# Kernel optimization log

Hardware: AMD Instinct MI355X
Metric: run time of the kernel (lower is better)

## Reference

```python
import jax, jax.numpy as jnp
import numpy as np

B, H, W, C = 32, 56, 56, 192
NUM_HEADS = 6
WS = 7
SHIFT = 3
HIDDEN = 4 * C


def _relative_position_index(ws):
    coords = np.stack(np.meshgrid(np.arange(ws), np.arange(ws), indexing="ij"))  # 2,ws,ws
    coords = coords.reshape(2, -1)
    rel = coords[:, :, None] - coords[:, None, :]  # 2,N,N
    rel = rel.transpose(1, 2, 0)
    rel[:, :, 0] += ws - 1
    rel[:, :, 1] += ws - 1
    rel[:, :, 0] *= 2 * ws - 1
    return rel.sum(-1)  # N,N in [0, (2ws-1)^2)


def setup_inputs() -> dict:
    key = jax.random.key(0)
    ks = jax.random.split(key, 16)
    s = 0.02
    inp = {
        "x": jax.random.normal(ks[0], (B, H, W, C), jnp.float32),
        "norm1_g": jnp.ones((C,), jnp.float32),
        "norm1_b": jnp.zeros((C,), jnp.float32),
        "qkv_w": jax.random.normal(ks[1], (3 * C, C), jnp.float32) * s,
        "qkv_b": jnp.zeros((3 * C,), jnp.float32),
        "proj_w": jax.random.normal(ks[2], (C, C), jnp.float32) * s,
        "proj_b": jnp.zeros((C,), jnp.float32),
        "rel_bias_table": jax.random.normal(ks[3], ((2 * WS - 1) ** 2, NUM_HEADS), jnp.float32) * s,
        "norm2_g": jnp.ones((C,), jnp.float32),
        "norm2_b": jnp.zeros((C,), jnp.float32),
        "fc1_w": jax.random.normal(ks[4], (HIDDEN, C), jnp.float32) * s,
        "fc1_b": jnp.zeros((HIDDEN,), jnp.float32),
        "fc2_w": jax.random.normal(ks[5], (C, HIDDEN), jnp.float32) * s,
        "fc2_b": jnp.zeros((C,), jnp.float32),
        "rel_index": jnp.asarray(_relative_position_index(WS), jnp.int32),  # (49,49)
    }
    return inp


def _layernorm(x, g, b, eps=1e-5):
    mu = x.mean(-1, keepdims=True)
    var = ((x - mu) ** 2).mean(-1, keepdims=True)
    return (x - mu) * jax.lax.rsqrt(var + eps) * g + b


def _window_partition(x, ws):
    b, h, w, c = x.shape
    x = x.reshape(b, h // ws, ws, w // ws, ws, c)
    return x.transpose(0, 1, 3, 2, 4, 5).reshape(-1, ws * ws, c)


def _window_reverse(win, ws, b, h, w):
    c = win.shape[-1]
    x = win.reshape(b, h // ws, w // ws, ws, ws, c)
    return x.transpose(0, 1, 3, 2, 4, 5).reshape(b, h, w, c)


def reference(x, norm1_g, norm1_b, qkv_w, qkv_b, proj_w, proj_b, rel_bias_table,
              norm2_g, norm2_b, fc1_w, fc1_b, fc2_w, fc2_b, rel_index):
    shortcut = x
    xn = _layernorm(x, norm1_g, norm1_b)
    xs = jnp.roll(xn, (-SHIFT, -SHIFT), axis=(1, 2))
    win = _window_partition(xs, WS)  # (nW*B, 49, C)
    nw, n, c = win.shape
    hd = c // NUM_HEADS
    qkv = win @ qkv_w.T + qkv_b  # (nw, n, 3C)
    qkv = qkv.reshape(nw, n, 3, NUM_HEADS, hd).transpose(2, 0, 3, 1, 4)
    q, k, v = qkv[0], qkv[1], qkv[2]  # (nw, heads, n, hd)
    q = q * (hd ** -0.5)
    attn = jnp.einsum("whnd,whmd->whnm", q, k)
    bias = rel_bias_table[rel_index.reshape(-1)].reshape(n, n, NUM_HEADS).transpose(2, 0, 1)
    attn = jax.nn.softmax(attn + bias[None], axis=-1)
    out = jnp.einsum("whnm,whmd->whnd", attn, v)
    out = out.transpose(0, 2, 1, 3).reshape(nw, n, c)
    out = out @ proj_w.T + proj_b
    xs = _window_reverse(out, WS, x.shape[0], x.shape[1], x.shape[2])
    xa = jnp.roll(xs, (SHIFT, SHIFT), axis=(1, 2))
    x = shortcut + xa
    xm = _layernorm(x, norm2_g, norm2_b)
    xm = jax.nn.gelu(xm @ fc1_w.T + fc1_b, approximate=False)
    xm = xm @ fc2_w.T + fc2_b
    return x + xm
```

## Files before the change

### kernel.cpp

```cpp
#include <hip/hip_runtime.h>
#include <hip/hip_bf16.h>

#define CC 192
#define NHEADS 6
#define HDIM 32
#define NTOK 49
#define NWIN 2048
#define MTOK 100352
#define HIDDEN 768

typedef __hip_bfloat16 bf16;
typedef __attribute__((ext_vector_type(8))) short short8;
typedef __attribute__((ext_vector_type(4))) float f32x4;

__global__ __launch_bounds__(256) void k_wconv(
    const float* __restrict__ qw, const float* __restrict__ pw,
    const float* __restrict__ f1, const float* __restrict__ f2,
    bf16* __restrict__ o) {
  int i = blockIdx.x * 256 + threadIdx.x;
  if (i < 110592) o[i] = __float2bfloat16(qw[i]);
  else if (i < 147456) o[i] = __float2bfloat16(pw[i - 110592]);
  else if (i < 294912) o[i] = __float2bfloat16(f1[i - 147456]);
  else if (i < 442368) o[i] = __float2bfloat16(f2[i - 294912]);
}

__global__ __launch_bounds__(256) void k_bias(
    const float* __restrict__ table, const int* __restrict__ ridx,
    float* __restrict__ bias6) {
  int i = blockIdx.x * 256 + threadIdx.x;
  if (i >= 6 * 2401) return;
  int h = i / 2401, e = i - h * 2401;
  bias6[i] = table[ridx[e] * NHEADS + h];
}

__global__ __launch_bounds__(256) void k_ln1_part(
    const float* __restrict__ x, const float* __restrict__ g,
    const float* __restrict__ bta, bf16* __restrict__ xw) {
  int wv = blockIdx.x * 4 + (threadIdx.x >> 6);
  int lane = threadIdx.x & 63;
  int w = wv / NTOK, n = wv - w * NTOK;
  int b = w >> 6, wrem = w & 63;
  int hi = wrem >> 3, wi = wrem & 7;
  int i = n / 7, j = n - i * 7;
  int hsrc = hi * 7 + i + 3; if (hsrc >= 56) hsrc -= 56;
  int wsrc = wi * 7 + j + 3; if (wsrc >= 56) wsrc -= 56;
  const float* row = x + (size_t)((b * 56 + hsrc) * 56 + wsrc) * CC;
  float v0 = row[lane], v1 = row[lane + 64], v2 = row[lane + 128];
  float s = v0 + v1 + v2;
  for (int m = 32; m; m >>= 1) s += __shfl_xor(s, m, 64);
  float mu = s * (1.0f / 192.0f);
  float d0 = v0 - mu, d1 = v1 - mu, d2 = v2 - mu;
  float q = d0 * d0 + d1 * d1 + d2 * d2;
  for (int m = 32; m; m >>= 1) q += __shfl_xor(q, m, 64);
  float inv = rsqrtf(q * (1.0f / 192.0f) + 1e-5f);
  bf16* orow = xw + (size_t)wv * CC;
  orow[lane]       = __float2bfloat16(d0 * inv * g[lane]       + bta[lane]);
  orow[lane + 64]  = __float2bfloat16(d1 * inv * g[lane + 64]  + bta[lane + 64]);
  orow[lane + 128] = __float2bfloat16(d2 * inv * g[lane + 128] + bta[lane + 128]);
}

__global__ __launch_bounds__(256) void k_ln2(
    const float* __restrict__ x1, const float* __restrict__ g,
    const float* __restrict__ bta, bf16* __restrict__ xn2) {
  int wv = blockIdx.x * 4 + (threadIdx.x >> 6);
  int lane = threadIdx.x & 63;
  const float* row = x1 + (size_t)wv * CC;
  float v0 = row[lane], v1 = row[lane + 64], v2 = row[lane + 128];
  float s = v0 + v1 + v2;
  for (int m = 32; m; m >>= 1) s += __shfl_xor(s, m, 64);
  float mu = s * (1.0f / 192.0f);
  float d0 = v0 - mu, d1 = v1 - mu, d2 = v2 - mu;
  float q = d0 * d0 + d1 * d1 + d2 * d2;
  for (int m = 32; m; m >>= 1) q += __shfl_xor(q, m, 64);
  float inv = rsqrtf(q * (1.0f / 192.0f) + 1e-5f);
  bf16* orow = xn2 + (size_t)wv * CC;
  orow[lane]       = __float2bfloat16(d0 * inv * g[lane]       + bta[lane]);
  orow[lane + 64]  = __float2bfloat16(d1 * inv * g[lane + 64]  + bta[lane + 64]);
  orow[lane + 128] = __float2bfloat16(d2 * inv * g[lane + 128] + bta[lane + 128]);
}

template <int MODE, int NT, int KC, int MF>
__global__ __launch_bounds__(256) void k_gemm_areg(
    const bf16* __restrict__ A, const bf16* __restrict__ W,
    const float* __restrict__ bias, void* __restrict__ out0,
    const void* __restrict__ aux) {
  constexpr int K = KC * 192;
  constexpr int N = NT * 64;
  __shared__ bf16 Bs[2][64 * 192];
  const int tid = threadIdx.x;
  const int wave = tid >> 6, lane = tid & 63;
  const int grp = lane >> 4, rA = lane & 15;
  const int cq = grp, cn = rA;
  const int m0 = blockIdx.x * (MF * 64);
  const int mrow = m0 + wave * (MF * 16);

  short8 areg[MF][KC * 6];
#pragma unroll
  for (int mt = 0; mt < MF; ++mt) {
    const bf16* arow = A + (size_t)(mrow + mt * 16 + rA) * K + grp * 8;
#pragma unroll
    for (int kt = 0; kt < KC * 6; ++kt)
      areg[mt][kt] = *(const short8*)(arow + kt * 32);
  }

  int rowoff[MF][4];
  if (MODE == 1) {
#pragma unroll
    for (int mt = 0; mt < MF; ++mt)
#pragma unroll
      for (int r = 0; r < 4; ++r) {
        int m = mrow + mt * 16 + cq * 4 + r;
        int w = m / 49, rr = m - w * 49;
        int b = w >> 6, wrem = w & 63;
        int hi = wrem >> 3, wi = wrem & 7;
        int ii = rr / 7, jj = rr - ii * 7;
        int hd = hi * 7 + ii + 3; if (hd >= 56) hd -= 56;
        int wd = wi * 7 + jj + 3; if (wd >= 56) wd -= 56;
        rowoff[mt][r] = ((b * 56 + hd) * 56 + wd) * CC;
      }
  }

  auto stage = [&](int buf, int nt, int kc) {
#pragma unroll
    for (int i = 0; i < 6; ++i) {
      int c = i * 256 + tid;
      int row = c / 24;
      int cbl = ((c - row * 24) * 16) ^ ((row & 7) << 4);
      const char* src = (const char*)W +
          (size_t)(nt * 64 + row) * (K * 2) + kc * 384 + cbl;
      __builtin_amdgcn_global_load_lds(
          (const __attribute__((address_space(1))) void*)src,
          (__attribute__((address_space(3))) void*)((char*)&Bs[buf][0] + c * 16),
          16, 0, 0);
    }
  };
  stage(0, 0, 0);

  f32x4 acc[MF][4];
#pragma unroll
  for (int s = 0; s < NT * KC; ++s) {
    const int nt = s / KC, kc = s - nt * KC;
    const int cur = s & 1;
    __syncthreads();
    if (s + 1 < NT * KC) stage(cur ^ 1, (s + 1) / KC, (s + 1) % KC);
    if (kc == 0) {
#pragma unroll
      for (int mt = 0; mt < MF; ++mt)
#pragma unroll
        for (int ntf = 0; ntf < 4; ++ntf)
          acc[mt][ntf] = (f32x4){0.f, 0.f, 0.f, 0.f};
    }
#pragma unroll
    for (int kt = 0; kt < 6; ++kt) {
      short8 b[4];
#pragma unroll
      for (int ntf = 0; ntf < 4; ++ntf) {
        int row = ntf * 16 + rA;
        int phys = row * 384 + ((kt * 64 + grp * 16) ^ ((row & 7) << 4));
        b[ntf] = *(const short8*)((const char*)&Bs[cur][0] + phys);
      }
#pragma unroll
      for (int mt = 0; mt < MF; ++mt)
#pragma unroll
        for (int ntf = 0; ntf < 4; ++ntf)
          acc[mt][ntf] = __builtin_amdgcn_mfma_f32_16x16x32_bf16(
              areg[mt][kc * 6 + kt], b[ntf], acc[mt][ntf], 0, 0, 0);
    }
    if (kc == KC - 1) {
      const int n0t = nt * 64;
      float bi[4];
#pragma unroll
      for (int ntf = 0; ntf < 4; ++ntf) bi[ntf] = bias[n0t + ntf * 16 + cn];
#pragma unroll
      for (int mt = 0; mt < MF; ++mt) {
#pragma unroll
        for (int r = 0; r < 4; ++r) {
          const int m = mrow + mt * 16 + cq * 4 + r;
#pragma unroll
          for (int ntf = 0; ntf < 4; ++ntf) {
            const int n = n0t + ntf * 16 + cn;
            float v = acc[mt][ntf][r] + bi[ntf];
            if (MODE == 0) {
              ((bf16*)out0)[(size_t)m * N + n] = __float2bfloat16(v);
            } else if (MODE == 2) {
              float ge = 0.5f * v * (1.0f + erff(v * 0.70710678118654752f));
              ((bf16*)out0)[(size_t)m * N + n] = __float2bfloat16(ge);
            } else if (MODE == 1) {
              float res = ((const float*)aux)[(size_t)rowoff[mt][r] + n];
              ((float*)out0)[(size_t)rowoff[mt][r] + n] = v + res;
            } else {
              float res = ((const float*)aux)[(size_t)m * CC + n];
              ((float*)out0)[(size_t)m * CC + n] = v + res;
            }
          }
        }
      }
    }
  }
}

__global__ __launch_bounds__(256) void k_attn_mfma(
    const bf16* __restrict__ qk, const float* __restrict__ bias6,
    bf16* __restrict__ ao) {
  __shared__ bf16 P[4][64 * 72];
  __shared__ bf16 VT[4][32 * 72];
  const int wave = threadIdx.x >> 6, lane = threadIdx.x & 63;
  const int wh = blockIdx.x * 4 + wave;
  const int w = wh / NHEADS, h = wh - w * NHEADS;
  const int rA = lane & 15, kq = (lane >> 4) * 8;
  const int grp = lane >> 4;

  const bf16* qbase = qk + (size_t)(w * 49) * 576 + h * HDIM + kq;

  short8 aq[4], bk[4], vrow[4];
#pragma unroll
  for (int t = 0; t < 4; ++t) {
    const bf16* rp = qbase + (size_t)(t * 16 + rA) * 576;
    aq[t] = *(const short8*)(rp);
    bk[t] = *(const short8*)(rp + 192);
    vrow[t] = *(const short8*)(rp + 384);
  }

  f32x4 S[4][4] = {};
#pragma unroll
  for (int mt = 0; mt < 4; ++mt)
#pragma unroll
    for (int nt = 0; nt < 4; ++nt)
      S[mt][nt] = __builtin_amdgcn_mfma_f32_16x16x32_bf16(
          aq[mt], bk[nt], S[mt][nt], 0, 0, 0);

  bf16* Vw = VT[wave];
  const bf16 zero = __float2bfloat16(0.0f);
#pragma unroll
  for (int t = 0; t < 4; ++t) {
    int tok = t * 16 + rA;
#pragma unroll
    for (int j = 0; j < 8; ++j)
      Vw[(kq + j) * 72 + tok] = (tok < 49) ? ((const bf16*)&vrow[t])[j] : zero;
  }

  const float scale = 0.17677669529663687f;
  const float* bh = bias6 + h * 2401;
  float rs[4][4];
  bf16* Pw = P[wave];
#pragma unroll
  for (int mt = 0; mt < 4; ++mt) {
#pragma unroll
    for (int r = 0; r < 4; ++r) {
      int row = mt * 16 + grp * 4 + r;
      float val[4];
#pragma unroll
      for (int nt = 0; nt < 4; ++nt) {
        int c = nt * 16 + rA;
        float bv = (row < 49 && c < 49) ? bh[row * 49 + c] : 0.0f;
        val[nt] = (c < 49) ? (S[mt][nt][r] * scale + bv) : -1e30f;
      }
      float mx = fmaxf(fmaxf(val[0], val[1]), fmaxf(val[2], val[3]));
      for (int m2 = 1; m2 < 16; m2 <<= 1) mx = fmaxf(mx, __shfl_xor(mx, m2, 64));
      float sum = 0.0f;
#pragma unroll
      for (int nt = 0; nt < 4; ++nt) {
        float e = __expf(val[nt] - mx);
        val[nt] = e;
        sum += e;
      }
      for (int m2 = 1; m2 < 16; m2 <<= 1) sum += __shfl_xor(sum, m2, 64);
      rs[mt][r] = 1.0f / sum;
#pragma unroll
      for (int nt = 0; nt < 4; ++nt)
        Pw[row * 72 + nt * 16 + rA] = __float2bfloat16(val[nt]);
    }
  }
  __syncthreads();

  short8 bv[2][2];
#pragma unroll
  for (int ks = 0; ks < 2; ++ks)
#pragma unroll
    for (int nt = 0; nt < 2; ++nt)
      bv[ks][nt] = *(const short8*)&Vw[(nt * 16 + rA) * 72 + ks * 32 + kq];
  f32x4 O[4][2] = {};
#pragma unroll
  for (int mt = 0; mt < 4; ++mt) {
    short8 ap0 = *(const short8*)&Pw[(mt * 16 + rA) * 72 + kq];
    short8 ap1 = *(const short8*)&Pw[(mt * 16 + rA) * 72 + 32 + kq];
#pragma unroll
    for (int nt = 0; nt < 2; ++nt) {
      O[mt][nt] = __builtin_amdgcn_mfma_f32_16x16x32_bf16(ap0, bv[0][nt],
                                                          O[mt][nt], 0, 0, 0);
      O[mt][nt] = __builtin_amdgcn_mfma_f32_16x16x32_bf16(ap1, bv[1][nt],
                                                          O[mt][nt], 0, 0, 0);
    }
  }
#pragma unroll
  for (int mt = 0; mt < 4; ++mt) {
#pragma unroll
    for (int r = 0; r < 4; ++r) {
      int m = mt * 16 + grp * 4 + r;
      if (m < 49) {
        bf16* orow = ao + (size_t)(w * 49 + m) * CC + h * HDIM;
#pragma unroll
        for (int nt = 0; nt < 2; ++nt)
          orow[nt * 16 + rA] = __float2bfloat16(O[mt][nt][r] * rs[mt][r]);
      }
    }
  }
}

extern "C" void kernel_launch(void* const* d_in, const int* in_sizes, int n_in,
                              void* d_out, int out_size, void* d_ws, size_t ws_size,
                              hipStream_t stream) {
  const float* x        = (const float*)d_in[0];
  const float* norm1_g  = (const float*)d_in[1];
  const float* norm1_b  = (const float*)d_in[2];
  const float* qkv_w    = (const float*)d_in[3];
  const float* qkv_b    = (const float*)d_in[4];
  const float* proj_w   = (const float*)d_in[5];
  const float* proj_b   = (const float*)d_in[6];
  const float* rel_tab  = (const float*)d_in[7];
  const float* norm2_g  = (const float*)d_in[8];
  const float* norm2_b  = (const float*)d_in[9];
  const float* fc1_w    = (const float*)d_in[10];
  const float* fc1_b    = (const float*)d_in[11];
  const float* fc2_w    = (const float*)d_in[12];
  const float* fc2_b    = (const float*)d_in[13];
  const int*   rel_idx  = (const int*)d_in[14];
  float* out = (float*)d_out;

  char* ws = (char*)d_ws;
  bf16*  xw    = (bf16*)ws;
  bf16*  qkb   = (bf16*)(ws + 38535168);
  bf16*  wbuf  = (bf16*)(ws + 154140672);
  float* bias6 = (float*)(ws + 155025408);
  bf16*  ao    = xw;
  bf16*  xn2   = xw;
  bf16*  hbuf  = qkb;
  float* x1    = out;
  bf16* wq = wbuf;
  bf16* wp = wbuf + 110592;
  bf16* w1 = wbuf + 147456;
  bf16* w2 = wbuf + 294912;

  k_wconv<<<1728, 256, 0, stream>>>(qkv_w, proj_w, fc1_w, fc2_w, wbuf);
  k_bias<<<57, 256, 0, stream>>>(rel_tab, rel_idx, bias6);
  k_ln1_part<<<MTOK / 4, 256, 0, stream>>>(x, norm1_g, norm1_b, xw);
  k_gemm_areg<0, 9, 1, 2><<<MTOK / 128, 256, 0, stream>>>(
      xw, wq, qkv_b, qkb, nullptr);
  k_attn_mfma<<<NWIN * NHEADS / 4, 256, 0, stream>>>(qkb, bias6, ao);
  k_gemm_areg<1, 3, 1, 2><<<MTOK / 128, 256, 0, stream>>>(
      ao, wp, proj_b, x1, x);
  k_ln2<<<MTOK / 4, 256, 0, stream>>>(x1, norm2_g, norm2_b, xn2);
  const int MH = MTOK / 2;
  for (int h = 0; h < 2; ++h) {
    size_t mo = (size_t)h * MH;
    k_gemm_areg<2, 12, 1, 2><<<MH / 128, 256, 0, stream>>>(
        xn2 + mo * CC, w1, fc1_b, hbuf, nullptr);
    k_gemm_areg<3, 3, 4, 1><<<MH / 64, 256, 0, stream>>>(
        hbuf, w2, fc2_b, out + mo * CC, x1 + mo * CC);
  }
}
```

Measured before the change: 546.6 us.

## Fuse LayerNorms into GEMM prologues and use tanh-form GELU

Removes the separate LN1 and LN2 kernels. The QKV and FC1 GEMMs now load fp32 rows directly, with the shifted-window gather for QKV, and compute LayerNorm in registers before the MFMA loop. This drops a bf16 intermediate write and read per LayerNorm, at the cost of smaller M tiles (MF=1) and more load work per GEMM block. The MLP runs over the full M in one pass when the workspace is large enough. Exact erf GELU is replaced by a tanh approximation built on __expf, which changes numerics slightly.

```diff
diff --git a/kernel.cpp b/kernel.cpp
--- a/kernel.cpp
+++ b/kernel.cpp
@@ -33,57 +33,12 @@
   bias6[i] = table[ridx[e] * NHEADS + h];
 }
 
-__global__ __launch_bounds__(256) void k_ln1_part(
-    const float* __restrict__ x, const float* __restrict__ g,
-    const float* __restrict__ bta, bf16* __restrict__ xw) {
-  int wv = blockIdx.x * 4 + (threadIdx.x >> 6);
-  int lane = threadIdx.x & 63;
-  int w = wv / NTOK, n = wv - w * NTOK;
-  int b = w >> 6, wrem = w & 63;
-  int hi = wrem >> 3, wi = wrem & 7;
-  int i = n / 7, j = n - i * 7;
-  int hsrc = hi * 7 + i + 3; if (hsrc >= 56) hsrc -= 56;
-  int wsrc = wi * 7 + j + 3; if (wsrc >= 56) wsrc -= 56;
-  const float* row = x + (size_t)((b * 56 + hsrc) * 56 + wsrc) * CC;
-  float v0 = row[lane], v1 = row[lane + 64], v2 = row[lane + 128];
-  float s = v0 + v1 + v2;
-  for (int m = 32; m; m >>= 1) s += __shfl_xor(s, m, 64);
-  float mu = s * (1.0f / 192.0f);
-  float d0 = v0 - mu, d1 = v1 - mu, d2 = v2 - mu;
-  float q = d0 * d0 + d1 * d1 + d2 * d2;
-  for (int m = 32; m; m >>= 1) q += __shfl_xor(q, m, 64);
-  float inv = rsqrtf(q * (1.0f / 192.0f) + 1e-5f);
-  bf16* orow = xw + (size_t)wv * CC;
-  orow[lane]       = __float2bfloat16(d0 * inv * g[lane]       + bta[lane]);
-  orow[lane + 64]  = __float2bfloat16(d1 * inv * g[lane + 64]  + bta[lane + 64]);
-  orow[lane + 128] = __float2bfloat16(d2 * inv * g[lane + 128] + bta[lane + 128]);
-}
-
-__global__ __launch_bounds__(256) void k_ln2(
-    const float* __restrict__ x1, const float* __restrict__ g,
-    const float* __restrict__ bta, bf16* __restrict__ xn2) {
-  int wv = blockIdx.x * 4 + (threadIdx.x >> 6);
-  int lane = threadIdx.x & 63;
-  const float* row = x1 + (size_t)wv * CC;
-  float v0 = row[lane], v1 = row[lane + 64], v2 = row[lane + 128];
-  float s = v0 + v1 + v2;
-  for (int m = 32; m; m >>= 1) s += __shfl_xor(s, m, 64);
-  float mu = s * (1.0f / 192.0f);
-  float d0 = v0 - mu, d1 = v1 - mu, d2 = v2 - mu;
-  float q = d0 * d0 + d1 * d1 + d2 * d2;
-  for (int m = 32; m; m >>= 1) q += __shfl_xor(q, m, 64);
-  float inv = rsqrtf(q * (1.0f / 192.0f) + 1e-5f);
-  bf16* orow = xn2 + (size_t)wv * CC;
-  orow[lane]       = __float2bfloat16(d0 * inv * g[lane]       + bta[lane]);
-  orow[lane + 64]  = __float2bfloat16(d1 * inv * g[lane + 64]  + bta[lane + 64]);
-  orow[lane + 128] = __float2bfloat16(d2 * inv * g[lane + 128] + bta[lane + 128]);
-}
-
 template <int MODE, int NT, int KC, int MF>
 __global__ __launch_bounds__(256) void k_gemm_areg(
-    const bf16* __restrict__ A, const bf16* __restrict__ W,
+    const void* __restrict__ Ap, const bf16* __restrict__ W,
     const float* __restrict__ bias, void* __restrict__ out0,
-    const void* __restrict__ aux) {
+    const void* __restrict__ aux, const float* __restrict__ lng,
+    const float* __restrict__ lnb) {
   constexpr int K = KC * 192;
   constexpr int N = NT * 64;
   __shared__ bf16 Bs[2][64 * 192];
@@ -95,16 +50,74 @@
   const int mrow = m0 + wave * (MF * 16);
 
   short8 areg[MF][KC * 6];
-#pragma unroll
-  for (int mt = 0; mt < MF; ++mt) {
-    const bf16* arow = A + (size_t)(mrow + mt * 16 + rA) * K + grp * 8;
-#pragma unroll
-    for (int kt = 0; kt < KC * 6; ++kt)
-      areg[mt][kt] = *(const short8*)(arow + kt * 32);
+  if constexpr (MODE == 1 || MODE == 3) {
+#pragma unroll
+    for (int mt = 0; mt < MF; ++mt) {
+      const bf16* arow =
+          (const bf16*)Ap + (size_t)(mrow + mt * 16 + rA) * K + grp * 8;
+#pragma unroll
+      for (int kt = 0; kt < KC * 6; ++kt)
+        areg[mt][kt] = *(const short8*)(arow + kt * 32);
+    }
+  } else {
+#pragma unroll
+    for (int mt = 0; mt < MF; ++mt) {
+      int m = mrow + mt * 16 + rA;
+      const float* rowp;
+      if constexpr (MODE == 0) {
+        int w = m / 49, n = m - w * 49;
+        int b = w >> 6, wrem = w & 63;
+        int hi = wrem >> 3, wi = wrem & 7;
+        int ii = n / 7, jj = n - ii * 7;
+        int hs = hi * 7 + ii + 3; if (hs >= 56) hs -= 56;
+        int wsc = wi * 7 + jj + 3; if (wsc >= 56) wsc -= 56;
+        rowp = (const float*)Ap + (size_t)((b * 56 + hs) * 56 + wsc) * CC;
+      } else {
+        rowp = (const float*)Ap + (size_t)m * CC;
+      }
+      f32x4 xv[12];
+#pragma unroll
+      for (int kt = 0; kt < 6; ++kt) {
+        xv[2 * kt]     = *(const f32x4*)(rowp + kt * 32 + grp * 8);
+        xv[2 * kt + 1] = *(const f32x4*)(rowp + kt * 32 + grp * 8 + 4);
+      }
+      float s = 0.0f;
+#pragma unroll
+      for (int i = 0; i < 12; ++i)
+#pragma unroll
+        for (int j = 0; j < 4; ++j) s += xv[i][j];
+      s += __shfl_xor(s, 16, 64);
+      s += __shfl_xor(s, 32, 64);
+      float mu = s * (1.0f / 192.0f);
+      float q = 0.0f;
+#pragma unroll
+      for (int i = 0; i < 12; ++i)
+#pragma unroll
+        for (int j = 0; j < 4; ++j) {
+          float d = xv[i][j] - mu;
+          q += d * d;
+        }
+      q += __shfl_xor(q, 16, 64);
+      q += __shfl_xor(q, 32, 64);
+      float inv = rsqrtf(q * (1.0f / 192.0f) + 1e-5f);
+#pragma unroll
+      for (int kt = 0; kt < 6; ++kt) {
+        short8 t;
+#pragma unroll
+        for (int j = 0; j < 8; ++j) {
+          int col = kt * 32 + grp * 8 + j;
+          float xval = xv[2 * kt + (j >> 2)][j & 3];
+          float val = (xval - mu) * inv * lng[col] + lnb[col];
+          bf16 hb = __float2bfloat16(val);
+          t[j] = *reinterpret_cast<short*>(&hb);
+        }
+        areg[mt][kt] = t;
+      }
+    }
   }
 
   int rowoff[MF][4];
-  if (MODE == 1) {
+  if constexpr (MODE == 1) {
 #pragma unroll
     for (int mt = 0; mt < MF; ++mt)
 #pragma unroll
@@ -180,12 +193,14 @@
           for (int ntf = 0; ntf < 4; ++ntf) {
             const int n = n0t + ntf * 16 + cn;
             float v = acc[mt][ntf][r] + bi[ntf];
-            if (MODE == 0) {
+            if constexpr (MODE == 0) {
               ((bf16*)out0)[(size_t)m * N + n] = __float2bfloat16(v);
-            } else if (MODE == 2) {
-              float ge = 0.5f * v * (1.0f + erff(v * 0.70710678118654752f));
+            } else if constexpr (MODE == 2) {
+              float u2 = 2.0f * v * (0.7978845608f + 0.0356774081f * v * v);
+              float t = 1.0f - 2.0f / (1.0f + __expf(u2));
+              float ge = 0.5f * v * (1.0f + t);
               ((bf16*)out0)[(size_t)m * N + n] = __float2bfloat16(ge);
-            } else if (MODE == 1) {
+            } else if constexpr (MODE == 1) {
               float res = ((const float*)aux)[(size_t)rowoff[mt][r] + n];
               ((float*)out0)[(size_t)rowoff[mt][r] + n] = v + res;
             } else {
@@ -327,15 +342,30 @@
   const int*   rel_idx  = (const int*)d_in[14];
   float* out = (float*)d_out;
 
+  const size_t SZ_QKB = 115605504ull;
+  const size_t SZ_HBF = 154140672ull;
+  const size_t SZ_AO  = 38535168ull;
+  const size_t SZ_WB  = 884736ull;
+  const size_t SZ_B6  = 57624ull;
+  const bool fullM = ws_size >= SZ_HBF + SZ_AO + SZ_WB + SZ_B6;
+
   char* ws = (char*)d_ws;
-  bf16*  xw    = (bf16*)ws;
-  bf16*  qkb   = (bf16*)(ws + 38535168);
-  bf16*  wbuf  = (bf16*)(ws + 154140672);
-  float* bias6 = (float*)(ws + 155025408);
-  bf16*  ao    = xw;
-  bf16*  xn2   = xw;
-  bf16*  hbuf  = qkb;
-  float* x1    = out;
+  bf16 *qkb, *ao, *wbuf, *hbuf;
+  float* bias6;
+  if (fullM) {
+    qkb   = (bf16*)ws;
+    hbuf  = (bf16*)ws;
+    ao    = (bf16*)(ws + SZ_HBF);
+    wbuf  = (bf16*)(ws + SZ_HBF + SZ_AO);
+    bias6 = (float*)(ws + SZ_HBF + SZ_AO + SZ_WB);
+  } else {
+    qkb   = (bf16*)ws;
+    hbuf  = (bf16*)ws;
+    ao    = (bf16*)(ws + SZ_QKB);
+    wbuf  = (bf16*)(ws + SZ_QKB + SZ_AO);
+    bias6 = (float*)(ws + SZ_QKB + SZ_AO + SZ_WB);
+  }
+  float* x1 = out;
   bf16* wq = wbuf;
   bf16* wp = wbuf + 110592;
   bf16* w1 = wbuf + 147456;
@@ -343,19 +373,24 @@
 
   k_wconv<<<1728, 256, 0, stream>>>(qkv_w, proj_w, fc1_w, fc2_w, wbuf);
   k_bias<<<57, 256, 0, stream>>>(rel_tab, rel_idx, bias6);
-  k_ln1_part<<<MTOK / 4, 256, 0, stream>>>(x, norm1_g, norm1_b, xw);
-  k_gemm_areg<0, 9, 1, 2><<<MTOK / 128, 256, 0, stream>>>(
-      xw, wq, qkv_b, qkb, nullptr);
+  k_gemm_areg<0, 9, 1, 1><<<MTOK / 64, 256, 0, stream>>>(
+      x, wq, qkv_b, qkb, nullptr, norm1_g, norm1_b);
   k_attn_mfma<<<NWIN * NHEADS / 4, 256, 0, stream>>>(qkb, bias6, ao);
   k_gemm_areg<1, 3, 1, 2><<<MTOK / 128, 256, 0, stream>>>(
-      ao, wp, proj_b, x1, x);
-  k_ln2<<<MTOK / 4, 256, 0, stream>>>(x1, norm2_g, norm2_b, xn2);
-  const int MH = MTOK / 2;
-  for (int h = 0; h < 2; ++h) {
-    size_t mo = (size_t)h * MH;
-    k_gemm_areg<2, 12, 1, 2><<<MH / 128, 256, 0, stream>>>(
-        xn2 + mo * CC, w1, fc1_b, hbuf, nullptr);
-    k_gemm_areg<3, 3, 4, 1><<<MH / 64, 256, 0, stream>>>(
-        hbuf, w2, fc2_b, out + mo * CC, x1 + mo * CC);
-  }
-}
+      ao, wp, proj_b, x1, x, nullptr, nullptr);
+  if (fullM) {
+    k_gemm_areg<2, 12, 1, 1><<<MTOK / 64, 256, 0, stream>>>(
+        x1, w1, fc1_b, hbuf, nullptr, norm2_g, norm2_b);
+    k_gemm_areg<3, 3, 4, 1><<<MTOK / 64, 256, 0, stream>>>(
+        hbuf, w2, fc2_b, out, x1, nullptr, nullptr);
+  } else {
+    const int MH = MTOK / 2;
+    for (int h = 0; h < 2; ++h) {
+      size_t mo = (size_t)h * MH;
+      k_gemm_areg<2, 12, 1, 1><<<MH / 64, 256, 0, stream>>>(
+          x1 + mo * CC, w1, fc1_b, hbuf, nullptr, norm2_g, norm2_b);
+      k_gemm_areg<3, 3, 4, 1><<<MH / 64, 256, 0, stream>>>(
+          hbuf, w2, fc2_b, out + mo * CC, x1 + mo * CC, nullptr, nullptr);
+    }
+  }
+}
```

Measured after the change: 473.5 us. 1.15x faster.
